# Kernel optimization log

Measured on AMD Instinct MI355X. Metric: run time of the kernel, lower is better.

Reference implementation:

```python
import jax, jax.numpy as jnp
import numpy as np

BEV_H = 128; BEV_W = 128; HEADS = 8; POINTS = 4; NUM_LAYERS = 6
PC = (-51.2, -51.2, -5.0, 51.2, 51.2, 3.0)
EPS = 1e-5


def _layernorm(x, g, b):
    m = x.mean(-1, keepdims=True)
    v = x.var(-1, keepdims=True)
    return (x - m) * jax.lax.rsqrt(v + 1e-5) * g + b


def _bilinear(feat, loc):
    # feat: (H, W, D); loc: (..., 2) normalized xy in [0, 1]; zero padding outside.
    H, W = feat.shape[0], feat.shape[1]
    ix = loc[..., 0] * W - 0.5
    iy = loc[..., 1] * H - 0.5
    x0 = jnp.floor(ix); y0 = jnp.floor(iy)
    fx = ix - x0; fy = iy - y0
    out = 0.0
    for dx in (0, 1):
        for dy in (0, 1):
            xi = x0 + dx; yi = y0 + dy
            w = (fx if dx else 1.0 - fx) * (fy if dy else 1.0 - fy)
            m = (xi >= 0) & (xi < W) & (yi >= 0) & (yi < H)
            xi_c = jnp.clip(xi, 0, W - 1).astype(jnp.int32)
            yi_c = jnp.clip(yi, 0, H - 1).astype(jnp.int32)
            out = out + (w * m)[..., None] * feat[yi_c, xi_c]
    return out


def _deform_grid(q, value, H, W, ref, ow, ob, aw, ab):
    # Deformable attention over a (H, W) grid of values; q: (Nq, C), value: (H*W, C).
    Nq, C = q.shape
    hd = C // HEADS
    v = value.reshape(H, W, HEADS, hd).transpose(2, 0, 1, 3)            # (h, H, W, hd)
    off = (q @ ow + ob).reshape(Nq, HEADS, POINTS, 2)
    loc = ref[:, None, None, :] + off / jnp.array([W, H], q.dtype)      # (Nq, h, P, 2)
    attn = jax.nn.softmax((q @ aw + ab).reshape(Nq, HEADS, POINTS), axis=-1)
    sampled = jax.vmap(_bilinear)(v, loc.transpose(1, 0, 2, 3))         # (h, Nq, P, hd)
    return jnp.einsum('hnpd,nhp->nhd', sampled, attn).reshape(Nq, C)


def _sca(q, feats, ref_cam, valid, ow, ob, aw, ab):
    # Spatial cross-attention: feats (Ncam, h, Hf, Wf, hd), ref_cam (Ncam, Nq, P, 2),
    # valid (Ncam, Nq, P) float mask of in-frustum projections.
    Nq, C = q.shape
    Hf, Wf = feats.shape[2], feats.shape[3]
    off = (q @ ow + ob).reshape(Nq, HEADS, POINTS, 2)
    loc = ref_cam[:, None] + (off / jnp.array([Wf, Hf], q.dtype)).transpose(1, 0, 2, 3)[None]
    # loc: (Ncam, h, Nq, P, 2)
    attn = jax.nn.softmax((q @ aw + ab).reshape(Nq, HEADS, POINTS), axis=-1)
    sampled = jax.vmap(jax.vmap(_bilinear))(feats, loc)                 # (Ncam, h, Nq, P, hd)
    num = jnp.einsum('chnpd,nhp,cnp->nhd', sampled, attn, valid)
    cnt = jnp.maximum(valid.sum((0, 2)), 1.0)                           # (Nq,)
    return (num / cnt[:, None, None]).reshape(Nq, C)


def _forward(image_feats, camera_intrinsics, camera_extrinsics, prev_bev, bev_embed,
             tsa_vw, tsa_vb, tsa_ow, tsa_ob, tsa_aw, tsa_ab, tsa_pw, tsa_pb,
             sca_vw, sca_vb, sca_ow, sca_ob, sca_aw, sca_ab, sca_pw, sca_pb,
             ffn_w1, ffn_b1, ffn_w2, ffn_b2,
             ln1_g, ln1_b, ln2_g, ln2_b, ln3_g, ln3_b):
    Ncam, C, Hf, Wf = image_feats.shape
    hd = C // HEADS
    Nq = BEV_H * BEV_W
    dt = image_feats.dtype
    feats_flat = image_feats.transpose(0, 2, 3, 1).reshape(Ncam * Hf * Wf, C)

    # 2D reference points for temporal self-attention (each query's own cell).
    xs = (jnp.arange(BEV_W, dtype=dt) + 0.5) / BEV_W
    ys = (jnp.arange(BEV_H, dtype=dt) + 0.5) / BEV_H
    gx, gy = jnp.meshgrid(xs, ys)                                       # (H, W) each
    ref2d = jnp.stack([gx.reshape(-1), gy.reshape(-1)], -1)             # (Nq, 2)

    # 3D pillar reference points projected into each camera.
    xm = PC[0] + gx.reshape(-1) * (PC[3] - PC[0])
    ym = PC[1] + gy.reshape(-1) * (PC[4] - PC[1])
    zm = PC[2] + (jnp.arange(POINTS, dtype=dt) + 0.5) / POINTS * (PC[5] - PC[2])
    ref3d = jnp.stack([
        jnp.broadcast_to(xm[:, None], (Nq, POINTS)),
        jnp.broadcast_to(ym[:, None], (Nq, POINTS)),
        jnp.broadcast_to(zm[None, :], (Nq, POINTS)),
        jnp.ones((Nq, POINTS), dt)], -1)                                # (Nq, P, 4)
    ego2cam = jnp.linalg.inv(camera_extrinsics[0])                      # (Ncam, 4, 4)
    pcam = jnp.einsum('cij,npj->cnpi', ego2cam, ref3d)[..., :3]
    img = jnp.einsum('cij,cnpj->cnpi', camera_intrinsics[0], pcam)
    z = img[..., 2]
    un = img[..., 0] / (jnp.maximum(z, EPS) * Wf)
    vn = img[..., 1] / (jnp.maximum(z, EPS) * Hf)
    valid = ((z > EPS) & (un >= 0) & (un <= 1) & (vn >= 0) & (vn <= 1)).astype(dt)
    ref_cam = jnp.stack([un, vn], -1)                                   # (Ncam, Nq, P, 2)

    q = bev_embed                                                       # (Nq, C)
    prev = prev_bev[:, 0, :]                                            # (Nq, C), B = 1
    for l in range(NUM_LAYERS):
        # Temporal self-attention: deformable sampling from prev BEV + current BEV.
        v_prev = prev @ tsa_vw[l] + tsa_vb[l]
        v_cur = q @ tsa_vw[l] + tsa_vb[l]
        a = 0.5 * (_deform_grid(q, v_prev, BEV_H, BEV_W, ref2d, tsa_ow[l], tsa_ob[l], tsa_aw[l], tsa_ab[l])
                   + _deform_grid(q, v_cur, BEV_H, BEV_W, ref2d, tsa_ow[l], tsa_ob[l], tsa_aw[l], tsa_ab[l]))
        q = _layernorm(q + a @ tsa_pw[l] + tsa_pb[l], ln1_g[l], ln1_b[l])
        # Spatial cross-attention over multi-camera image features.
        v_img = (feats_flat @ sca_vw[l] + sca_vb[l]).reshape(Ncam, Hf, Wf, HEADS, hd).transpose(0, 3, 1, 2, 4)
        a = _sca(q, v_img, ref_cam, valid, sca_ow[l], sca_ob[l], sca_aw[l], sca_ab[l])
        q = _layernorm(q + a @ sca_pw[l] + sca_pb[l], ln2_g[l], ln2_b[l])
        # FFN
        a = jax.nn.relu(q @ ffn_w1[l] + ffn_b1[l]) @ ffn_w2[l] + ffn_b2[l]
        q = _layernorm(q + a, ln3_g[l], ln3_b[l])
    return q.T.reshape(1, C, BEV_H, BEV_W)


def setup_inputs() -> dict:
    key = jax.random.key(0)
    ks = iter(jax.random.split(key, 80))
    def nrm(shape, s=0.02):
        return jax.random.normal(next(ks), shape, jnp.float32) * s
    C, L, Ncam, Hf, Wf = 256, NUM_LAYERS, 6, 58, 100
    Nq = BEV_H * BEV_W
    HP, HP2 = HEADS * POINTS, HEADS * POINTS * 2
    # Structured nuScenes-like cameras: 6 yaws at 60 deg, intrinsics at feature-map scale.
    extr = np.zeros((1, Ncam, 4, 4), np.float32)
    for c in range(Ncam):
        t = c * np.pi / 3.0
        f = np.array([np.cos(t), np.sin(t), 0.0])
        xc = np.array([np.sin(t), -np.cos(t), 0.0])
        yc = np.array([0.0, 0.0, -1.0])
        extr[0, c, :3, :3] = np.stack([xc, yc, f], axis=1)
        extr[0, c, :3, 3] = 1.5 * f + np.array([0.0, 0.0, 1.5])
        extr[0, c, 3, 3] = 1.0
    intr = np.zeros((1, Ncam, 3, 3), np.float32)
    intr[0, :, 0, 0] = 80.0; intr[0, :, 1, 1] = 80.0
    intr[0, :, 0, 2] = Wf / 2.0; intr[0, :, 1, 2] = Hf / 2.0
    intr[0, :, 2, 2] = 1.0
    return {
        'image_feats': jax.random.normal(next(ks), (Ncam, C, Hf, Wf), jnp.float32),
        'camera_intrinsics': jnp.asarray(intr),
        'camera_extrinsics': jnp.asarray(extr),
        'prev_bev': jax.random.normal(next(ks), (Nq, 1, C), jnp.float32),
        'bev_embed': nrm((Nq, C)),
        'tsa_vw': nrm((L, C, C)), 'tsa_vb': jnp.zeros((L, C), jnp.float32),
        'tsa_ow': nrm((L, C, HP2)), 'tsa_ob': nrm((L, HP2), 2.0),
        'tsa_aw': nrm((L, C, HP)), 'tsa_ab': jnp.zeros((L, HP), jnp.float32),
        'tsa_pw': nrm((L, C, C)), 'tsa_pb': jnp.zeros((L, C), jnp.float32),
        'sca_vw': nrm((L, C, C)), 'sca_vb': jnp.zeros((L, C), jnp.float32),
        'sca_ow': nrm((L, C, HP2)), 'sca_ob': nrm((L, HP2), 2.0),
        'sca_aw': nrm((L, C, HP)), 'sca_ab': jnp.zeros((L, HP), jnp.float32),
        'sca_pw': nrm((L, C, C)), 'sca_pb': jnp.zeros((L, C), jnp.float32),
        'ffn_w1': nrm((L, C, 2 * C)), 'ffn_b1': jnp.zeros((L, 2 * C), jnp.float32),
        'ffn_w2': nrm((L, 2 * C, C)), 'ffn_b2': jnp.zeros((L, C), jnp.float32),
        'ln1_g': jnp.ones((L, C), jnp.float32), 'ln1_b': jnp.zeros((L, C), jnp.float32),
        'ln2_g': jnp.ones((L, C), jnp.float32), 'ln2_b': jnp.zeros((L, C), jnp.float32),
        'ln3_g': jnp.ones((L, C), jnp.float32), 'ln3_b': jnp.zeros((L, C), jnp.float32),
    }


def reference(image_feats, camera_intrinsics, camera_extrinsics, prev_bev, bev_embed,
              tsa_vw, tsa_vb, tsa_ow, tsa_ob, tsa_aw, tsa_ab, tsa_pw, tsa_pb,
              sca_vw, sca_vb, sca_ow, sca_ob, sca_aw, sca_ab, sca_pw, sca_pb,
              ffn_w1, ffn_b1, ffn_w2, ffn_b2,
              ln1_g, ln1_b, ln2_g, ln2_b, ln3_g, ln3_b):
    return _forward(image_feats, camera_intrinsics, camera_extrinsics, prev_bev, bev_embed,
                    tsa_vw, tsa_vb, tsa_ow, tsa_ob, tsa_aw, tsa_ab, tsa_pw, tsa_pb,
                    sca_vw, sca_vb, sca_ow, sca_ob, sca_aw, sca_ab, sca_pw, sca_pb,
                    ffn_w1, ffn_b1, ffn_w2, ffn_b2,
                    ln1_g, ln1_b, ln2_g, ln2_b, ln3_g, ln3_b)
```

## Files before the change

### kernel.cpp

```cpp
#include <hip/hip_runtime.h>
#include <hip/hip_bf16.h>
#include <math.h>

typedef __hip_bfloat16 bf16;

#define NQ      16384
#define CDIM    256
#define NHEADS  8
#define NPOINTS 4
#define NCAM    6
#define HF      58
#define WF      100
#define HWF     (HF*WF)
#define NFEAT   (NCAM*HWF)
#define HD      32
#define NLAYERS 6

typedef __attribute__((ext_vector_type(8))) short short8;
typedef __attribute__((ext_vector_type(4))) float floatx4;

__device__ __forceinline__ float toF(float x) { return x; }
__device__ __forceinline__ float toF(bf16 x) { return __bfloat162float(x); }
__device__ __forceinline__ void storeD(float* p, float v) { *p = v; }
__device__ __forceinline__ void storeD(bf16* p, float v) { *p = __float2bfloat16(v); }

__device__ __forceinline__ float bfLo(unsigned u) { return __uint_as_float(u << 16); }
__device__ __forceinline__ float bfHi(unsigned u) { return __uint_as_float(u & 0xffff0000u); }

__device__ __forceinline__ void gload_lds16(const bf16* g, bf16* l) {
    __builtin_amdgcn_global_load_lds(
        (const __attribute__((address_space(1))) void*)(g),
        (__attribute__((address_space(3))) void*)(l), 16, 0, 0);
}


template <typename DT, bool RELU, bool STAGE, bool ZF>
__global__ __launch_bounds__(256) void gemm_mfma(
    const bf16* __restrict__ A, const bf16* __restrict__ BT,
    const float* __restrict__ bias, DT* __restrict__ D,
    int M, int N, int K, size_t sB, size_t sBias, size_t sD)
{
    int z, bn;
    if (ZF) {
        z  = blockIdx.x % NLAYERS;
        bn = (blockIdx.x / NLAYERS) * 128;
    } else {
        z  = blockIdx.z;
        bn = blockIdx.x * 128;
    }
    BT += (size_t)z * sB;
    bias += (size_t)z * sBias;
    D += (size_t)z * sD;

    __shared__ bf16 smem[STAGE ? 128 * 136 : 128 * 64];
    bf16* As = smem;
    bf16* Bs = smem + 128 * 32;

    int tid = threadIdx.x;
    int lane = tid & 63, w = tid >> 6;
    int wm = w & 1, wn = w >> 1;
    int l15 = lane & 15, quad = lane >> 4;
    int bm = blockIdx.y * 128;

    floatx4 acc[4][4];
#pragma unroll
    for (int i = 0; i < 4; i++)
#pragma unroll
        for (int j = 0; j < 4; j++)
            acc[i][j] = (floatx4){0.f, 0.f, 0.f, 0.f};

    int rsub = lane >> 2;
    int kc   = (((lane & 3) ^ ((rsub >> 1) & 3))) * 8;
    int sw   = (l15 >> 1) & 3;

    for (int k0 = 0; k0 < K; k0 += 32) {
#pragma unroll
        for (int h = 0; h < 2; h++) {
            int r0 = w * 32 + h * 16;
            int gm = bm + r0 + rsub;
            if (gm > M - 1) gm = M - 1;
            gload_lds16(A + (size_t)gm * K + k0 + kc, &As[r0 * 32]);
            gload_lds16(BT + (size_t)(bn + r0 + rsub) * K + k0 + kc, &Bs[r0 * 32]);
        }
        __syncthreads();

        short8 a[4], b[4];
#pragma unroll
        for (int i = 0; i < 4; i++)
            a[i] = *(const short8*)(&As[(wm * 64 + i * 16 + l15) * 32 + (quad ^ sw) * 8]);
#pragma unroll
        for (int j = 0; j < 4; j++)
            b[j] = *(const short8*)(&Bs[(wn * 64 + j * 16 + l15) * 32 + (quad ^ sw) * 8]);
#pragma unroll
        for (int i = 0; i < 4; i++)
#pragma unroll
            for (int j = 0; j < 4; j++)
                acc[i][j] = __builtin_amdgcn_mfma_f32_16x16x32_bf16(
                    a[i], b[j], acc[i][j], 0, 0, 0);
        __syncthreads();
    }

    if (STAGE) {
#pragma unroll
        for (int i = 0; i < 4; i++) {
#pragma unroll
            for (int j = 0; j < 4; j++) {
                int col = wn * 64 + j * 16 + l15;
                float bv = bias[bn + col];
#pragma unroll
                for (int r = 0; r < 4; r++) {
                    int row = wm * 64 + i * 16 + quad * 4 + r;
                    float v = acc[i][j][r] + bv;
                    if (RELU) v = fmaxf(v, 0.f);
                    smem[row * 136 + col] = __float2bfloat16(v);
                }
            }
        }
        __syncthreads();
        int lr0 = tid >> 4;
        int ck  = tid & 15;
#pragma unroll
        for (int pass = 0; pass < 8; pass++) {
            int lr = pass * 16 + lr0;
            int gm = bm + lr;
            if (gm < M) {
                uint4 v = *(const uint4*)(&smem[lr * 136 + ck * 8]);
                *(uint4*)((bf16*)D + (size_t)gm * N + bn + ck * 8) = v;
            }
        }
    } else {
#pragma unroll
        for (int i = 0; i < 4; i++) {
#pragma unroll
            for (int j = 0; j < 4; j++) {
                int col = bn + wn * 64 + j * 16 + l15;
                float bv = bias[col];
#pragma unroll
                for (int r = 0; r < 4; r++) {
                    int row = bm + wm * 64 + i * 16 + quad * 4 + r;
                    if (row < M) {
                        float v = acc[i][j][r] + bv;
                        if (RELU) v = fmaxf(v, 0.f);
                        storeD(&D[(size_t)row * N + col], v);
                    }
                }
            }
        }
    }
}

__global__ __launch_bounds__(256) void gemm_off(
    const bf16* __restrict__ A, const bf16* __restrict__ BT,
    const float* __restrict__ bias, float* __restrict__ D)
{
    __shared__ bf16 As[64 * 32];
    __shared__ bf16 Bs[64 * 32];

    int tid = threadIdx.x;
    int lane = tid & 63, w = tid >> 6;
    int l15 = lane & 15, quad = lane >> 4;
    int bm = blockIdx.y * 64, bn = blockIdx.x * 64;

    floatx4 acc[4];
#pragma unroll
    for (int j = 0; j < 4; j++)
        acc[j] = (floatx4){0.f, 0.f, 0.f, 0.f};

    int rsub = lane >> 2;
    int kc   = (((lane & 3) ^ ((rsub >> 1) & 3))) * 8;
    int sw   = (l15 >> 1) & 3;

    for (int k0 = 0; k0 < 256; k0 += 32) {
        gload_lds16(A + (size_t)(bm + w * 16 + rsub) * 256 + k0 + kc, &As[w * 16 * 32]);
        gload_lds16(BT + (size_t)(bn + w * 16 + rsub) * 256 + k0 + kc, &Bs[w * 16 * 32]);
        __syncthreads();

        short8 a = *(const short8*)(&As[(w * 16 + l15) * 32 + (quad ^ sw) * 8]);
        short8 b[4];
#pragma unroll
        for (int j = 0; j < 4; j++)
            b[j] = *(const short8*)(&Bs[(j * 16 + l15) * 32 + (quad ^ sw) * 8]);
#pragma unroll
        for (int j = 0; j < 4; j++)
            acc[j] = __builtin_amdgcn_mfma_f32_16x16x32_bf16(a, b[j], acc[j], 0, 0, 0);
        __syncthreads();
    }

#pragma unroll
    for (int j = 0; j < 4; j++) {
        int col = bn + j * 16 + l15;
        float bv = bias[col];
#pragma unroll
        for (int r = 0; r < 4; r++) {
            int row = bm + w * 16 + quad * 4 + r;
            D[(size_t)row * 128 + col] = acc[j][r] + bv;
        }
    }
}

__global__ __launch_bounds__(256) void gemm_tsa(
    const bf16* __restrict__ A, const bf16* __restrict__ BT,
    const float* __restrict__ bias,
    bf16* __restrict__ vgrid, float* __restrict__ offlog)
{
    int bn3 = blockIdx.x;
    int bm = blockIdx.y * 128;
    if (bn3 == 2 && bm < NQ) return;
    int bn = bn3 * 128;

    __shared__ bf16 As[128 * 32];
    __shared__ bf16 Bs[128 * 32];

    int tid = threadIdx.x;
    int lane = tid & 63, w = tid >> 6;
    int wm = w & 1, wn = w >> 1;
    int l15 = lane & 15, quad = lane >> 4;

    floatx4 acc[4][4];
#pragma unroll
    for (int i = 0; i < 4; i++)
#pragma unroll
        for (int j = 0; j < 4; j++)
            acc[i][j] = (floatx4){0.f, 0.f, 0.f, 0.f};

    int rsub = lane >> 2;
    int kc   = (((lane & 3) ^ ((rsub >> 1) & 3))) * 8;
    int sw   = (l15 >> 1) & 3;

    for (int k0 = 0; k0 < 256; k0 += 32) {
#pragma unroll
        for (int h = 0; h < 2; h++) {
            int r0 = w * 32 + h * 16;
            gload_lds16(A + (size_t)(bm + r0 + rsub) * 256 + k0 + kc, &As[r0 * 32]);
            gload_lds16(BT + (size_t)(bn + r0 + rsub) * 256 + k0 + kc, &Bs[r0 * 32]);
        }
        __syncthreads();

        short8 a[4], b[4];
#pragma unroll
        for (int i = 0; i < 4; i++)
            a[i] = *(const short8*)(&As[(wm * 64 + i * 16 + l15) * 32 + (quad ^ sw) * 8]);
#pragma unroll
        for (int j = 0; j < 4; j++)
            b[j] = *(const short8*)(&Bs[(wn * 64 + j * 16 + l15) * 32 + (quad ^ sw) * 8]);
#pragma unroll
        for (int i = 0; i < 4; i++)
#pragma unroll
            for (int j = 0; j < 4; j++)
                acc[i][j] = __builtin_amdgcn_mfma_f32_16x16x32_bf16(
                    a[i], b[j], acc[i][j], 0, 0, 0);
        __syncthreads();
    }

#pragma unroll
    for (int i = 0; i < 4; i++) {
#pragma unroll
        for (int j = 0; j < 4; j++) {
            int col = bn + wn * 64 + j * 16 + l15;
            float bv = bias[col];
#pragma unroll
            for (int r = 0; r < 4; r++) {
                int row = bm + wm * 64 + i * 16 + quad * 4 + r;
                float v = acc[i][j][r] + bv;
                if (bn3 < 2) {
                    int n = row & (NQ - 1);
                    int cur = row >= NQ;
                    size_t idx = ((size_t)n * 64 + (col >> 2)) * 8 + cur * 4 + (col & 3);
                    vgrid[idx] = __float2bfloat16(v);
                } else {
                    offlog[(size_t)(row - NQ) * 128 + (col - 256)] = v;
                }
            }
        }
    }
}

__global__ __launch_bounds__(512) void gemm_ln(
    const bf16* __restrict__ A, const bf16* __restrict__ BT,
    const float* __restrict__ bias,
    bf16* __restrict__ qb,
    const float* __restrict__ g, const float* __restrict__ b,
    int K)
{
    __shared__ bf16 As[64 * 32];
    __shared__ bf16 Bs[256 * 32];
    __shared__ float red[2][64][4];
    __shared__ float stats[2][64];

    int tid = threadIdx.x;
    int lane = tid & 63, w = tid >> 6;
    int wm = w & 1, wn = w >> 1;
    int l15 = lane & 15, quad = lane >> 4;
    int bm = blockIdx.x * 64;

    floatx4 acc[2][4];
#pragma unroll
    for (int i = 0; i < 2; i++)
#pragma unroll
        for (int j = 0; j < 4; j++)
            acc[i][j] = (floatx4){0.f, 0.f, 0.f, 0.f};

    int rsub = lane >> 2;
    int kc   = (((lane & 3) ^ ((rsub >> 1) & 3))) * 8;
    int sw   = (l15 >> 1) & 3;

    for (int k0 = 0; k0 < K; k0 += 32) {
#pragma unroll
        for (int h = 0; h < 2; h++) {
            int r0 = w * 32 + h * 16;
            gload_lds16(BT + (size_t)(r0 + rsub) * K + k0 + kc, &Bs[r0 * 32]);
        }
        if (w < 4)
            gload_lds16(A + (size_t)(bm + w * 16 + rsub) * K + k0 + kc,
                        &As[w * 16 * 32]);
        __syncthreads();

        short8 a[2], bfr[4];
#pragma unroll
        for (int i = 0; i < 2; i++)
            a[i] = *(const short8*)(&As[(wm * 32 + i * 16 + l15) * 32 + (quad ^ sw) * 8]);
#pragma unroll
        for (int j = 0; j < 4; j++)
            bfr[j] = *(const short8*)(&Bs[(wn * 64 + j * 16 + l15) * 32 + (quad ^ sw) * 8]);
#pragma unroll
        for (int i = 0; i < 2; i++)
#pragma unroll
            for (int j = 0; j < 4; j++)
                acc[i][j] = __builtin_amdgcn_mfma_f32_16x16x32_bf16(
                    a[i], bfr[j], acc[i][j], 0, 0, 0);
        __syncthreads();
    }

    float x[2][4][4];
#pragma unroll
    for (int i = 0; i < 2; i++) {
#pragma unroll
        for (int j = 0; j < 4; j++) {
            int col = wn * 64 + j * 16 + l15;
            float bv = bias[col];
#pragma unroll
            for (int r = 0; r < 4; r++) {
                int row = bm + wm * 32 + i * 16 + quad * 4 + r;
                x[i][j][r] = toF(qb[(size_t)row * CDIM + col]) + acc[i][j][r] + bv;
            }
        }
    }
#pragma unroll
    for (int i = 0; i < 2; i++) {
#pragma unroll
        for (int r = 0; r < 4; r++) {
            float s = x[i][0][r] + x[i][1][r] + x[i][2][r] + x[i][3][r];
            float sq = x[i][0][r] * x[i][0][r] + x[i][1][r] * x[i][1][r] +
                       x[i][2][r] * x[i][2][r] + x[i][3][r] * x[i][3][r];
#pragma unroll
            for (int m = 1; m < 16; m <<= 1) {
                s += __shfl_xor(s, m);
                sq += __shfl_xor(sq, m);
            }
            if (l15 == 0) {
                int rl = wm * 32 + i * 16 + quad * 4 + r;
                red[0][rl][wn] = s;
                red[1][rl][wn] = sq;
            }
        }
    }
    __syncthreads();
    if (tid < 64) {
        float s = red[0][tid][0] + red[0][tid][1] + red[0][tid][2] + red[0][tid][3];
        float sq = red[1][tid][0] + red[1][tid][1] + red[1][tid][2] + red[1][tid][3];
        float mean = s * (1.f / CDIM);
        float var = fmaxf(sq * (1.f / CDIM) - mean * mean, 0.f);
        stats[0][tid] = mean;
        stats[1][tid] = rsqrtf(var + 1e-5f);
    }
    __syncthreads();
#pragma unroll
    for (int i = 0; i < 2; i++) {
#pragma unroll
        for (int j = 0; j < 4; j++) {
            int col = wn * 64 + j * 16 + l15;
            float gc = g[col], bc = b[col];
#pragma unroll
            for (int r = 0; r < 4; r++) {
                int rl = wm * 32 + i * 16 + quad * 4 + r;
                int row = bm + rl;
                float y = (x[i][j][r] - stats[0][rl]) * stats[1][rl] * gc + bc;
                qb[(size_t)row * CDIM + col] = __float2bfloat16(y);
            }
        }
    }
}

__global__ void wt_cvt_kernel(const float* __restrict__ W, bf16* __restrict__ WT,
                              int K, int N)
{
    __shared__ float tile[32][33];
    int l = blockIdx.z;
    const float* Wl = W + (size_t)l * K * N;
    bf16* WTl = WT + (size_t)l * K * N;
    int k0 = blockIdx.x * 32, n0 = blockIdx.y * 32;
    int tx = threadIdx.x, ty = threadIdx.y;
    for (int i = 0; i < 32; i += 8)
        tile[ty + i][tx] = Wl[(size_t)(k0 + ty + i) * N + n0 + tx];
    __syncthreads();
    for (int i = 0; i < 32; i += 8)
        WTl[(size_t)(n0 + ty + i) * K + k0 + tx] = __float2bfloat16(tile[tx][ty + i]);
}

__global__ void pack_tsa_kernel(const float* __restrict__ vw, const float* __restrict__ vb,
                                const float* __restrict__ ow, const float* __restrict__ ob,
                                const float* __restrict__ aw, const float* __restrict__ ab,
                                bf16* __restrict__ WT, float* __restrict__ BIAS)
{
    int n = blockIdx.x;
    int l = blockIdx.y;
    int k = threadIdx.x;
    float v = 0.f;
    if (n < 256)      v = vw[((size_t)l * 256 + k) * 256 + n];
    else if (n < 320) v = ow[((size_t)l * 256 + k) * 64 + (n - 256)];
    else if (n < 352) v = aw[((size_t)l * 256 + k) * 32 + (n - 320)];
    WT[((size_t)l * 384 + n) * 256 + k] = __float2bfloat16(v);
    if (k == 0) {
        float bv = 0.f;
        if (n < 256)      bv = vb[l * 256 + n];
        else if (n < 320) bv = ob[l * 64 + (n - 256)];
        else if (n < 352) bv = ab[l * 32 + (n - 320)];
        BIAS[l * 384 + n] = bv;
    }
}

__global__ void pack_offattn_kernel(const float* __restrict__ ow, const float* __restrict__ ob,
                                    const float* __restrict__ aw, const float* __restrict__ ab,
                                    bf16* __restrict__ WT, float* __restrict__ BIAS)
{
    int l = blockIdx.y;
    int n = blockIdx.x;
    int k = threadIdx.x;
    float v = 0.f;
    if (n < 64)      v = ow[((size_t)l * 256 + k) * 64 + n];
    else if (n < 96) v = aw[((size_t)l * 256 + k) * 32 + (n - 64)];
    WT[((size_t)l * 128 + n) * 256 + k] = __float2bfloat16(v);
    if (k == 0) {
        float bv = 0.f;
        if (n < 64)      bv = ob[l * 64 + n];
        else if (n < 96) bv = ab[l * 32 + (n - 64)];
        BIAS[l * 128 + n] = bv;
    }
}

__global__ void feats_cvt_kernel(const float* __restrict__ in, bf16* __restrict__ outT)
{
    __shared__ float tile[32][33];
    int c = blockIdx.z;
    int r0 = blockIdx.x * 32, ch0 = blockIdx.y * 32;
    int tx = threadIdx.x, ty = threadIdx.y;
    for (int i = 0; i < 32; i += 8) {
        int r = r0 + tx, ch = ch0 + ty + i;
        tile[ty + i][tx] = (r < HWF) ? in[((size_t)c * CDIM + ch) * HWF + r] : 0.f;
    }
    __syncthreads();
    for (int i = 0; i < 32; i += 8) {
        int r = r0 + ty + i, ch = ch0 + tx;
        if (r < HWF)
            outT[((size_t)c * HWF + r) * CDIM + ch] = __float2bfloat16(tile[tx][ty + i]);
    }
}

__global__ __launch_bounds__(256) void cvt_bf16_kernel(const float* __restrict__ in,
                                                       bf16* __restrict__ out, int n)
{
    int i = blockIdx.x * 256 + threadIdx.x;
    if (i < n) out[i] = __float2bfloat16(in[i]);
}

__global__ void invert4_kernel(const float* __restrict__ extr, float* __restrict__ ego)
{
    int c = threadIdx.x;
    if (c >= NCAM) return;
    float a[4][8];
    for (int i = 0; i < 4; i++)
        for (int j = 0; j < 4; j++) {
            a[i][j] = extr[c * 16 + i * 4 + j];
            a[i][4 + j] = (i == j) ? 1.f : 0.f;
        }
    for (int col = 0; col < 4; col++) {
        int piv = col;
        float best = fabsf(a[col][col]);
        for (int r = col + 1; r < 4; r++) {
            float v = fabsf(a[r][col]);
            if (v > best) { best = v; piv = r; }
        }
        if (piv != col)
            for (int j = 0; j < 8; j++) {
                float t = a[col][j]; a[col][j] = a[piv][j]; a[piv][j] = t;
            }
        float inv = 1.f / a[col][col];
        for (int j = 0; j < 8; j++) a[col][j] *= inv;
        for (int r = 0; r < 4; r++) {
            if (r == col) continue;
            float f = a[r][col];
            for (int j = 0; j < 8; j++) a[r][j] -= f * a[col][j];
        }
    }
    for (int i = 0; i < 4; i++)
        for (int j = 0; j < 4; j++)
            ego[c * 16 + i * 4 + j] = a[i][4 + j];
}

__global__ __launch_bounds__(256) void refcam_kernel(
    const float* __restrict__ ego, const float* __restrict__ intr,
    float* __restrict__ refcam, float* __restrict__ validb)
{
    int t = blockIdx.x * 256 + threadIdx.x;
    if (t >= NCAM * NQ * NPOINTS) return;
    int p = t & 3;
    int n = (t >> 2) & (NQ - 1);
    int c = t >> 16;

    float gx = ((n & 127) + 0.5f) / 128.0f;
    float gy = ((n >> 7) + 0.5f) / 128.0f;
    float xm = -51.2f + gx * 102.4f;
    float ym = -51.2f + gy * 102.4f;
    float zm = -5.0f + (p + 0.5f) * 2.0f;

    const float* E = ego + c * 16;
    float pc[3];
#pragma unroll
    for (int i = 0; i < 3; i++)
        pc[i] = E[i * 4 + 0] * xm + E[i * 4 + 1] * ym + E[i * 4 + 2] * zm + E[i * 4 + 3];

    const float* I = intr + c * 9;
    float im[3];
#pragma unroll
    for (int i = 0; i < 3; i++)
        im[i] = I[i * 3 + 0] * pc[0] + I[i * 3 + 1] * pc[1] + I[i * 3 + 2] * pc[2];

    float z = im[2];
    float zc = fmaxf(z, 1e-5f);
    float un = im[0] / (zc * (float)WF);
    float vn = im[1] / (zc * (float)HF);
    float val = (z > 1e-5f && un >= 0.f && un <= 1.f && vn >= 0.f && vn <= 1.f) ? 1.f : 0.f;

    size_t idx = ((size_t)c * NQ + n) * NPOINTS + p;
    refcam[idx * 2] = un;
    refcam[idx * 2 + 1] = vn;
    validb[idx] = val;
}

__global__ __launch_bounds__(256) void tsa_sample_kernel(
    const bf16* __restrict__ vgrid, const float* __restrict__ offlog,
    bf16* __restrict__ outA)
{
    int blk = blockIdx.x;
    int qq = (blk & 7) * 512 + (blk >> 3);
    int t = threadIdx.x;
    int n = qq * 4 + (t >> 6);
    int r = t & 63;
    int h = r >> 3;
    int dq = r & 7;
    int col = h * HD + dq * 4;
    int q8 = h * 8 + dq;

    const float* fl = offlog + (size_t)n * 128;
    const float* lg = fl + 64 + h * 4;
    float l0 = lg[0], l1 = lg[1], l2 = lg[2], l3 = lg[3];
    float mx = fmaxf(fmaxf(l0, l1), fmaxf(l2, l3));
    float e0 = expf(l0 - mx), e1 = expf(l1 - mx), e2 = expf(l2 - mx), e3 = expf(l3 - mx);
    float inv = 1.f / (e0 + e1 + e2 + e3);
    float w[4] = { e0 * inv, e1 * inv, e2 * inv, e3 * inv };

    const float* of = fl + h * 8;
    float rx = ((n & 127) + 0.5f) / 128.f;
    float ry = ((n >> 7) + 0.5f) / 128.f;

    float a0 = 0.f, a1 = 0.f, a2 = 0.f, a3 = 0.f;
#pragma unroll
    for (int p = 0; p < NPOINTS; p++) {
        float lx = rx + of[p * 2] * (1.f / 128.f);
        float ly = ry + of[p * 2 + 1] * (1.f / 128.f);
        float ix = lx * 128.f - 0.5f;
        float iy = ly * 128.f - 0.5f;
        float xf = floorf(ix), yf = floorf(iy);
        float fx = ix - xf, fy = iy - yf;
        int x0 = (int)xf, y0 = (int)yf;
#pragma unroll
        for (int dy = 0; dy < 2; dy++) {
            int yi = y0 + dy;
            if (yi < 0 || yi >= 128) continue;
            float wy = dy ? fy : 1.f - fy;
#pragma unroll
            for (int dx = 0; dx < 2; dx++) {
                int xi = x0 + dx;
                if (xi < 0 || xi >= 128) continue;
                float wgt = w[p] * wy * (dx ? fx : 1.f - fx);
                size_t idx = ((size_t)(yi * 128 + xi) * 64 + q8) * 8;
                uint4 v = *(const uint4*)(vgrid + idx);
                a0 += wgt * (bfLo(v.x) + bfLo(v.z));
                a1 += wgt * (bfHi(v.x) + bfHi(v.z));
                a2 += wgt * (bfLo(v.y) + bfLo(v.w));
                a3 += wgt * (bfHi(v.y) + bfHi(v.w));
            }
        }
    }
    union { bf16 b[4]; uint2 u; } pk;
    pk.b[0] = __float2bfloat16(0.5f * a0);
    pk.b[1] = __float2bfloat16(0.5f * a1);
    pk.b[2] = __float2bfloat16(0.5f * a2);
    pk.b[3] = __float2bfloat16(0.5f * a3);
    *(uint2*)(outA + (size_t)n * CDIM + col) = pk.u;
}

__global__ __launch_bounds__(256) void sca_sample_kernel(
    const bf16* __restrict__ vimg, const float* __restrict__ offlog,
    const float* __restrict__ refcam, const float* __restrict__ validb,
    bf16* __restrict__ outA)
{
    int blk = blockIdx.x;
    int qo = (blk & 7) * 256 + (blk >> 3);
    int t = threadIdx.x;
    int n = qo * 8 + (t >> 5);
    int r = t & 31;
    int h = r >> 2;
    int d8 = r & 3;
    int col = h * HD + d8 * 8;

    const float* fl = offlog + (size_t)n * 128;
    const float* lg = fl + 64 + h * 4;
    float l0 = lg[0], l1 = lg[1], l2 = lg[2], l3 = lg[3];
    float mx = fmaxf(fmaxf(l0, l1), fmaxf(l2, l3));
    float e0 = expf(l0 - mx), e1 = expf(l1 - mx), e2 = expf(l2 - mx), e3 = expf(l3 - mx);
    float inv = 1.f / (e0 + e1 + e2 + e3);
    float w[4] = { e0 * inv, e1 * inv, e2 * inv, e3 * inv };

    const float* of = fl + h * 8;
    float ox[4], oy[4];
#pragma unroll
    for (int p = 0; p < NPOINTS; p++) {
        ox[p] = of[p * 2] * (1.f / (float)WF);
        oy[p] = of[p * 2 + 1] * (1.f / (float)HF);
    }

    float a0 = 0.f, a1 = 0.f, a2 = 0.f, a3 = 0.f;
    float a4 = 0.f, a5 = 0.f, a6 = 0.f, a7 = 0.f;
    float vsum = 0.f;
    for (int c = 0; c < NCAM; c++) {
        const bf16* vb = vimg + (size_t)c * HWF * CDIM;
        size_t base = ((size_t)c * NQ + n) * NPOINTS;
#pragma unroll
        for (int p = 0; p < NPOINTS; p++) {
            float vl = validb[base + p];
            vsum += vl;
            if (vl == 0.f) continue;
            float lx = refcam[(base + p) * 2] + ox[p];
            float ly = refcam[(base + p) * 2 + 1] + oy[p];
            float ix = lx * (float)WF - 0.5f;
            float iy = ly * (float)HF - 0.5f;
            float xf = floorf(ix), yf = floorf(iy);
            float fx = ix - xf, fy = iy - yf;
            int x0 = (int)xf, y0 = (int)yf;
            float wp_ = w[p] * vl;
#pragma unroll
            for (int dy = 0; dy < 2; dy++) {
                int yi = y0 + dy;
                if (yi < 0 || yi >= HF) continue;
                float wy = dy ? fy : 1.f - fy;
#pragma unroll
                for (int dx = 0; dx < 2; dx++) {
                    int xi = x0 + dx;
                    if (xi < 0 || xi >= WF) continue;
                    float wgt = wp_ * wy * (dx ? fx : 1.f - fx);
                    uint4 u = *(const uint4*)(vb + (size_t)(yi * WF + xi) * CDIM + col);
                    a0 += wgt * bfLo(u.x);
                    a1 += wgt * bfHi(u.x);
                    a2 += wgt * bfLo(u.y);
                    a3 += wgt * bfHi(u.y);
                    a4 += wgt * bfLo(u.z);
                    a5 += wgt * bfHi(u.z);
                    a6 += wgt * bfLo(u.w);
                    a7 += wgt * bfHi(u.w);
                }
            }
        }
    }
    float ic = 1.f / fmaxf(vsum, 1.f);
    union { bf16 b[8]; uint4 u; } pk;
    pk.b[0] = __float2bfloat16(a0 * ic);
    pk.b[1] = __float2bfloat16(a1 * ic);
    pk.b[2] = __float2bfloat16(a2 * ic);
    pk.b[3] = __float2bfloat16(a3 * ic);
    pk.b[4] = __float2bfloat16(a4 * ic);
    pk.b[5] = __float2bfloat16(a5 * ic);
    pk.b[6] = __float2bfloat16(a6 * ic);
    pk.b[7] = __float2bfloat16(a7 * ic);
    *(uint4*)(outA + (size_t)n * CDIM + col) = pk.u;
}

__global__ void out_transpose_kernel(const bf16* __restrict__ qb, float* __restrict__ out)
{
    __shared__ float tile[32][33];
    int n0 = blockIdx.x * 32;
    int c0 = blockIdx.y * 32;
    int tx = threadIdx.x, ty = threadIdx.y;
    for (int i = 0; i < 32; i += 8)
        tile[ty + i][tx] = toF(qb[(size_t)(n0 + ty + i) * CDIM + c0 + tx]);
    __syncthreads();
    for (int i = 0; i < 32; i += 8)
        out[(size_t)(c0 + ty + i) * NQ + n0 + tx] = tile[tx][ty + i];
}

extern "C" void kernel_launch(void* const* d_in, const int* in_sizes, int n_in,
                              void* d_out, int out_size, void* d_ws, size_t ws_size,
                              hipStream_t stream)
{
    const float* image_feats = (const float*)d_in[0];
    const float* intr        = (const float*)d_in[1];
    const float* extr        = (const float*)d_in[2];
    const float* prev_bev    = (const float*)d_in[3];
    const float* bev_embed   = (const float*)d_in[4];
    const float* tsa_vw = (const float*)d_in[5];
    const float* tsa_vb = (const float*)d_in[6];
    const float* tsa_ow = (const float*)d_in[7];
    const float* tsa_ob = (const float*)d_in[8];
    const float* tsa_aw = (const float*)d_in[9];
    const float* tsa_ab = (const float*)d_in[10];
    const float* tsa_pw = (const float*)d_in[11];
    const float* tsa_pb = (const float*)d_in[12];
    const float* sca_vw = (const float*)d_in[13];
    const float* sca_vb = (const float*)d_in[14];
    const float* sca_ow = (const float*)d_in[15];
    const float* sca_ob = (const float*)d_in[16];
    const float* sca_aw = (const float*)d_in[17];
    const float* sca_ab = (const float*)d_in[18];
    const float* sca_pw = (const float*)d_in[19];
    const float* sca_pb = (const float*)d_in[20];
    const float* ffn_w1 = (const float*)d_in[21];
    const float* ffn_b1 = (const float*)d_in[22];
    const float* ffn_w2 = (const float*)d_in[23];
    const float* ffn_b2 = (const float*)d_in[24];
    const float* ln1_g  = (const float*)d_in[25];
    const float* ln1_b  = (const float*)d_in[26];
    const float* ln2_g  = (const float*)d_in[27];
    const float* ln2_b  = (const float*)d_in[28];
    const float* ln3_g  = (const float*)d_in[29];
    const float* ln3_b  = (const float*)d_in[30];

    char* wp = (char*)d_ws;
    auto alloc = [&](size_t bytes) -> void* {
        void* r = (void*)wp;
        wp += (bytes + 255) & ~(size_t)255;
        return r;
    };
    bf16*  prevbf = (bf16*) alloc((size_t)NQ * CDIM * 2);
    bf16*  qb     = (bf16*) alloc((size_t)NQ * CDIM * 2);
    bf16*  attnA  = (bf16*) alloc((size_t)NQ * CDIM * 2);
    float* offlog = (float*)alloc((size_t)NQ * 128 * 4);
    float* refcam = (float*)alloc((size_t)NCAM * NQ * NPOINTS * 2 * 4);
    float* validb = (float*)alloc((size_t)NCAM * NQ * NPOINTS * 4);
    float* ego    = (float*)alloc(128 * 4);
    bf16*  featsT = (bf16*) alloc((size_t)NFEAT * CDIM * 2);
    bf16*  pwT  = (bf16*)alloc((size_t)NLAYERS * 65536 * 2);
    bf16*  svwT = (bf16*)alloc((size_t)NLAYERS * 65536 * 2);
    bf16*  spwT = (bf16*)alloc((size_t)NLAYERS * 65536 * 2);
    bf16*  w1T  = (bf16*)alloc((size_t)NLAYERS * 131072 * 2);
    bf16*  w2T  = (bf16*)alloc((size_t)NLAYERS * 131072 * 2);
    bf16*  ptwT = (bf16*)alloc((size_t)NLAYERS * 384 * 256 * 2);
    float* ptb  = (float*)alloc((size_t)NLAYERS * 384 * 4);
    bf16*  sowT = (bf16*)alloc((size_t)NLAYERS * 32768 * 2);
    float* sobF = (float*)alloc((size_t)NLAYERS * 128 * 4);
    bf16*  vgrid = (bf16*)alloc((size_t)NQ * CDIM * 2 * 2);
    bf16*  vimg6 = (bf16*)alloc((size_t)NLAYERS * NFEAT * CDIM * 2);

    bf16* hidden = featsT;

    dim3 blk32(32, 8);

    cvt_bf16_kernel<<<(NQ * CDIM + 255) / 256, 256, 0, stream>>>(bev_embed, qb, NQ * CDIM);
    cvt_bf16_kernel<<<(NQ * CDIM + 255) / 256, 256, 0, stream>>>(prev_bev, prevbf, NQ * CDIM);
    invert4_kernel<<<1, 64, 0, stream>>>(extr, ego);
    refcam_kernel<<<(NCAM * NQ * NPOINTS + 255) / 256, 256, 0, stream>>>(ego, intr, refcam, validb);
    {
        dim3 g((HWF + 31) / 32, CDIM / 32, NCAM);
        feats_cvt_kernel<<<g, blk32, 0, stream>>>(image_feats, featsT);
    }
    wt_cvt_kernel<<<dim3(8, 8,  NLAYERS), blk32, 0, stream>>>(tsa_pw, pwT,  256, 256);
    wt_cvt_kernel<<<dim3(8, 8,  NLAYERS), blk32, 0, stream>>>(sca_vw, svwT, 256, 256);
    wt_cvt_kernel<<<dim3(8, 8,  NLAYERS), blk32, 0, stream>>>(sca_pw, spwT, 256, 256);
    wt_cvt_kernel<<<dim3(8, 16, NLAYERS), blk32, 0, stream>>>(ffn_w1, w1T, 256, 512);
    wt_cvt_kernel<<<dim3(16, 8, NLAYERS), blk32, 0, stream>>>(ffn_w2, w2T, 512, 256);
    pack_tsa_kernel<<<dim3(384, NLAYERS), 256, 0, stream>>>(
        tsa_vw, tsa_vb, tsa_ow, tsa_ob, tsa_aw, tsa_ab, ptwT, ptb);
    pack_offattn_kernel<<<dim3(128, NLAYERS), 256, 0, stream>>>(
        sca_ow, sca_ob, sca_aw, sca_ab, sowT, sobF);
    gemm_mfma<bf16, false, true, true><<<dim3(2 * NLAYERS, (NFEAT + 127) / 128, 1), 256, 0, stream>>>(
        featsT, svwT, sca_vb, vimg6, NFEAT, CDIM, CDIM,
        65536, 256, (size_t)NFEAT * CDIM);

    for (int l = 0; l < NLAYERS; l++) {
        gemm_tsa<<<dim3(3, 2 * NQ / 128), 256, 0, stream>>>(
            prevbf, ptwT + (size_t)l * 98304, ptb + l * 384, vgrid, offlog);
        tsa_sample_kernel<<<NQ / 4, 256, 0, stream>>>(vgrid, offlog, attnA);
        gemm_ln<<<NQ / 64, 512, 0, stream>>>(
            attnA, pwT + (size_t)l * 65536, tsa_pb + l * CDIM,
            qb, ln1_g + l * CDIM, ln1_b + l * CDIM, CDIM);

        gemm_off<<<dim3(2, NQ / 64), 256, 0, stream>>>(
            qb, sowT + (size_t)l * 32768, sobF + l * 128, offlog);
        sca_sample_kernel<<<NQ / 8, 256, 0, stream>>>(
            vimg6 + (size_t)l * NFEAT * CDIM, offlog, refcam, validb, attnA);
        gemm_ln<<<NQ / 64, 512, 0, stream>>>(
            attnA, spwT + (size_t)l * 65536, sca_pb + l * CDIM,
            qb, ln2_g + l * CDIM, ln2_b + l * CDIM, CDIM);

        gemm_mfma<bf16, true, true, false><<<dim3(4, NQ / 128, 1), 256, 0, stream>>>(
            qb, w1T + (size_t)l * 131072, ffn_b1 + l * 512, hidden, NQ, 512, CDIM, 0, 0, 0);
        gemm_ln<<<NQ / 64, 512, 0, stream>>>(
            hidden, w2T + (size_t)l * 131072, ffn_b2 + l * CDIM,
            qb, ln3_g + l * CDIM, ln3_b + l * CDIM, 512);
    }

    {
        dim3 g(NQ / 32, CDIM / 32);
        out_transpose_kernel<<<g, blk32, 0, stream>>>(qb, (float*)d_out);
    }
}
```

Before: 993.3 us.

## Compact valid camera projections per query and remap feature-GEMM blocks across XCDs

```diff
diff --git a/kernel.cpp b/kernel.cpp
--- a/kernel.cpp
+++ b/kernel.cpp
@@ -40,13 +40,18 @@
     const float* __restrict__ bias, DT* __restrict__ D,
     int M, int N, int K, size_t sB, size_t sBias, size_t sD)
 {
-    int z, bn;
+    int z, bn, bm;
     if (ZF) {
-        z  = blockIdx.x % NLAYERS;
-        bn = (blockIdx.x / NLAYERS) * 128;
+        int nwg = gridDim.x;
+        int logical = (blockIdx.x & 7) * (nwg >> 3) + (blockIdx.x >> 3);
+        int idx = logical % (2 * NLAYERS);
+        bm = (logical / (2 * NLAYERS)) * 128;
+        z  = idx % NLAYERS;
+        bn = (idx / NLAYERS) * 128;
     } else {
         z  = blockIdx.z;
         bn = blockIdx.x * 128;
+        bm = blockIdx.y * 128;
     }
     BT += (size_t)z * sB;
     bias += (size_t)z * sBias;
@@ -60,7 +65,6 @@
     int lane = tid & 63, w = tid >> 6;
     int wm = w & 1, wn = w >> 1;
     int l15 = lane & 15, quad = lane >> 4;
-    int bm = blockIdx.y * 128;
 
     floatx4 acc[4][4];
 #pragma unroll
@@ -507,44 +511,45 @@
             ego[c * 16 + i * 4 + j] = a[i][4 + j];
 }
 
-__global__ __launch_bounds__(256) void refcam_kernel(
+__global__ __launch_bounds__(256) void refcam_compact_kernel(
     const float* __restrict__ ego, const float* __restrict__ intr,
-    float* __restrict__ refcam, float* __restrict__ validb)
-{
-    int t = blockIdx.x * 256 + threadIdx.x;
-    if (t >= NCAM * NQ * NPOINTS) return;
-    int p = t & 3;
-    int n = (t >> 2) & (NQ - 1);
-    int c = t >> 16;
+    float4* __restrict__ entries, int* __restrict__ cnt)
+{
+    int n = blockIdx.x * 256 + threadIdx.x;
+    if (n >= NQ) return;
 
     float gx = ((n & 127) + 0.5f) / 128.0f;
     float gy = ((n >> 7) + 0.5f) / 128.0f;
     float xm = -51.2f + gx * 102.4f;
     float ym = -51.2f + gy * 102.4f;
-    float zm = -5.0f + (p + 0.5f) * 2.0f;
-
-    const float* E = ego + c * 16;
-    float pc[3];
-#pragma unroll
-    for (int i = 0; i < 3; i++)
-        pc[i] = E[i * 4 + 0] * xm + E[i * 4 + 1] * ym + E[i * 4 + 2] * zm + E[i * 4 + 3];
-
-    const float* I = intr + c * 9;
-    float im[3];
-#pragma unroll
-    for (int i = 0; i < 3; i++)
-        im[i] = I[i * 3 + 0] * pc[0] + I[i * 3 + 1] * pc[1] + I[i * 3 + 2] * pc[2];
-
-    float z = im[2];
-    float zc = fmaxf(z, 1e-5f);
-    float un = im[0] / (zc * (float)WF);
-    float vn = im[1] / (zc * (float)HF);
-    float val = (z > 1e-5f && un >= 0.f && un <= 1.f && vn >= 0.f && vn <= 1.f) ? 1.f : 0.f;
-
-    size_t idx = ((size_t)c * NQ + n) * NPOINTS + p;
-    refcam[idx * 2] = un;
-    refcam[idx * 2 + 1] = vn;
-    validb[idx] = val;
+
+    float4* out = entries + (size_t)n * 24;
+    int k = 0;
+    for (int c = 0; c < NCAM; c++) {
+        const float* E = ego + c * 16;
+        const float* I = intr + c * 9;
+#pragma unroll
+        for (int p = 0; p < NPOINTS; p++) {
+            float zm = -5.0f + (p + 0.5f) * 2.0f;
+            float pc[3];
+#pragma unroll
+            for (int i = 0; i < 3; i++)
+                pc[i] = E[i * 4 + 0] * xm + E[i * 4 + 1] * ym + E[i * 4 + 2] * zm + E[i * 4 + 3];
+            float im[3];
+#pragma unroll
+            for (int i = 0; i < 3; i++)
+                im[i] = I[i * 3 + 0] * pc[0] + I[i * 3 + 1] * pc[1] + I[i * 3 + 2] * pc[2];
+            float z = im[2];
+            float zc = fmaxf(z, 1e-5f);
+            float un = im[0] / (zc * (float)WF);
+            float vn = im[1] / (zc * (float)HF);
+            if (z > 1e-5f && un >= 0.f && un <= 1.f && vn >= 0.f && vn <= 1.f) {
+                out[k] = make_float4(un, vn, __int_as_float(c * 4 + p), 0.f);
+                k++;
+            }
+        }
+    }
+    cnt[n] = k;
 }
 
 __global__ __launch_bounds__(256) void tsa_sample_kernel(
@@ -612,7 +617,7 @@
 
 __global__ __launch_bounds__(256) void sca_sample_kernel(
     const bf16* __restrict__ vimg, const float* __restrict__ offlog,
-    const float* __restrict__ refcam, const float* __restrict__ validb,
+    const float4* __restrict__ entries, const int* __restrict__ cnt,
     bf16* __restrict__ outA)
 {
     int blk = blockIdx.x;
@@ -640,49 +645,47 @@
         oy[p] = of[p * 2 + 1] * (1.f / (float)HF);
     }
 
+    int ne = cnt[n];
+    const float4* ent = entries + (size_t)n * 24;
+
     float a0 = 0.f, a1 = 0.f, a2 = 0.f, a3 = 0.f;
     float a4 = 0.f, a5 = 0.f, a6 = 0.f, a7 = 0.f;
-    float vsum = 0.f;
-    for (int c = 0; c < NCAM; c++) {
+    for (int e = 0; e < ne; e++) {
+        float4 E = ent[e];
+        int cp = __float_as_int(E.z);
+        int c = cp >> 2, p = cp & 3;
+        float lx = E.x + ox[p];
+        float ly = E.y + oy[p];
+        float ix = lx * (float)WF - 0.5f;
+        float iy = ly * (float)HF - 0.5f;
+        float xf = floorf(ix), yf = floorf(iy);
+        float fx = ix - xf, fy = iy - yf;
+        int x0 = (int)xf, y0 = (int)yf;
+        float wp_ = w[p];
         const bf16* vb = vimg + (size_t)c * HWF * CDIM;
-        size_t base = ((size_t)c * NQ + n) * NPOINTS;
-#pragma unroll
-        for (int p = 0; p < NPOINTS; p++) {
-            float vl = validb[base + p];
-            vsum += vl;
-            if (vl == 0.f) continue;
-            float lx = refcam[(base + p) * 2] + ox[p];
-            float ly = refcam[(base + p) * 2 + 1] + oy[p];
-            float ix = lx * (float)WF - 0.5f;
-            float iy = ly * (float)HF - 0.5f;
-            float xf = floorf(ix), yf = floorf(iy);
-            float fx = ix - xf, fy = iy - yf;
-            int x0 = (int)xf, y0 = (int)yf;
-            float wp_ = w[p] * vl;
-#pragma unroll
-            for (int dy = 0; dy < 2; dy++) {
-                int yi = y0 + dy;
-                if (yi < 0 || yi >= HF) continue;
-                float wy = dy ? fy : 1.f - fy;
-#pragma unroll
-                for (int dx = 0; dx < 2; dx++) {
-                    int xi = x0 + dx;
-                    if (xi < 0 || xi >= WF) continue;
-                    float wgt = wp_ * wy * (dx ? fx : 1.f - fx);
-                    uint4 u = *(const uint4*)(vb + (size_t)(yi * WF + xi) * CDIM + col);
-                    a0 += wgt * bfLo(u.x);
-                    a1 += wgt * bfHi(u.x);
-                    a2 += wgt * bfLo(u.y);
-                    a3 += wgt * bfHi(u.y);
-                    a4 += wgt * bfLo(u.z);
-                    a5 += wgt * bfHi(u.z);
-                    a6 += wgt * bfLo(u.w);
-                    a7 += wgt * bfHi(u.w);
-                }
-            }
-        }
-    }
-    float ic = 1.f / fmaxf(vsum, 1.f);
+#pragma unroll
+        for (int dy = 0; dy < 2; dy++) {
+            int yi = y0 + dy;
+            if (yi < 0 || yi >= HF) continue;
+            float wy = dy ? fy : 1.f - fy;
+#pragma unroll
+            for (int dx = 0; dx < 2; dx++) {
+                int xi = x0 + dx;
+                if (xi < 0 || xi >= WF) continue;
+                float wgt = wp_ * wy * (dx ? fx : 1.f - fx);
+                uint4 u = *(const uint4*)(vb + (size_t)(yi * WF + xi) * CDIM + col);
+                a0 += wgt * bfLo(u.x);
+                a1 += wgt * bfHi(u.x);
+                a2 += wgt * bfLo(u.y);
+                a3 += wgt * bfHi(u.y);
+                a4 += wgt * bfLo(u.z);
+                a5 += wgt * bfHi(u.z);
+                a6 += wgt * bfLo(u.w);
+                a7 += wgt * bfHi(u.w);
+            }
+        }
+    }
+    float ic = 1.f / fmaxf((float)ne, 1.f);
     union { bf16 b[8]; uint4 u; } pk;
     pk.b[0] = __float2bfloat16(a0 * ic);
     pk.b[1] = __float2bfloat16(a1 * ic);
@@ -754,8 +757,8 @@
     bf16*  qb     = (bf16*) alloc((size_t)NQ * CDIM * 2);
     bf16*  attnA  = (bf16*) alloc((size_t)NQ * CDIM * 2);
     float* offlog = (float*)alloc((size_t)NQ * 128 * 4);
-    float* refcam = (float*)alloc((size_t)NCAM * NQ * NPOINTS * 2 * 4);
-    float* validb = (float*)alloc((size_t)NCAM * NQ * NPOINTS * 4);
+    float4* entries = (float4*)alloc((size_t)NQ * 24 * 16);
+    int*   entcnt = (int*)  alloc((size_t)NQ * 4);
     float* ego    = (float*)alloc(128 * 4);
     bf16*  featsT = (bf16*) alloc((size_t)NFEAT * CDIM * 2);
     bf16*  pwT  = (bf16*)alloc((size_t)NLAYERS * 65536 * 2);
@@ -777,7 +780,7 @@
     cvt_bf16_kernel<<<(NQ * CDIM + 255) / 256, 256, 0, stream>>>(bev_embed, qb, NQ * CDIM);
     cvt_bf16_kernel<<<(NQ * CDIM + 255) / 256, 256, 0, stream>>>(prev_bev, prevbf, NQ * CDIM);
     invert4_kernel<<<1, 64, 0, stream>>>(extr, ego);
-    refcam_kernel<<<(NCAM * NQ * NPOINTS + 255) / 256, 256, 0, stream>>>(ego, intr, refcam, validb);
+    refcam_compact_kernel<<<NQ / 256, 256, 0, stream>>>(ego, intr, entries, entcnt);
     {
         dim3 g((HWF + 31) / 32, CDIM / 32, NCAM);
         feats_cvt_kernel<<<g, blk32, 0, stream>>>(image_feats, featsT);
@@ -791,7 +794,7 @@
         tsa_vw, tsa_vb, tsa_ow, tsa_ob, tsa_aw, tsa_ab, ptwT, ptb);
     pack_offattn_kernel<<<dim3(128, NLAYERS), 256, 0, stream>>>(
         sca_ow, sca_ob, sca_aw, sca_ab, sowT, sobF);
-    gemm_mfma<bf16, false, true, true><<<dim3(2 * NLAYERS, (NFEAT + 127) / 128, 1), 256, 0, stream>>>(
+    gemm_mfma<bf16, false, true, true><<<dim3(2 * NLAYERS * 272), 256, 0, stream>>>(
         featsT, svwT, sca_vb, vimg6, NFEAT, CDIM, CDIM,
         65536, 256, (size_t)NFEAT * CDIM);
 
@@ -806,7 +809,7 @@
         gemm_off<<<dim3(2, NQ / 64), 256, 0, stream>>>(
             qb, sowT + (size_t)l * 32768, sobF + l * 128, offlog);
         sca_sample_kernel<<<NQ / 8, 256, 0, stream>>>(
-            vimg6 + (size_t)l * NFEAT * CDIM, offlog, refcam, validb, attnA);
+            vimg6 + (size_t)l * NFEAT * CDIM, offlog, entries, entcnt, attnA);
         gemm_ln<<<NQ / 64, 512, 0, stream>>>(
             attnA, spwT + (size_t)l * 65536, sca_pb + l * CDIM,
             qb, ln2_g + l * CDIM, ln2_b + l * CDIM, CDIM);
```

Result: no change. 978.1 us (-1.5%).
